# Performance work log

Measured on AMD Instinct MI355X. Metric: run time of the kernel, lower is better.

Reference implementation:

```python
import jax, jax.numpy as jnp
import numpy as np

D = 384      # d_model
NH = 8       # num_heads
HW = 96      # spatial h = w
RATIOS = (4, 8, 16)


def _p2i(x):
    # (hg wg b) c h w -> b c (hg h) (wg w), hg=wg=2, b=1
    f, c, h, w = x.shape
    return x.reshape(2, 2, c, h, w).transpose(2, 0, 3, 1, 4).reshape(1, c, 2 * h, 2 * w)


def _i2p(x):
    # b c (hg h) (wg w) -> (hg wg b) c h w, hg=wg=2, b=1
    _, c, H2, W2 = x.shape
    h, w = H2 // 2, W2 // 2
    return x.reshape(c, 2, h, 2, w).transpose(1, 3, 0, 2, 4).reshape(4, c, h, w)


def _ln(x, g, b, eps=1e-5):
    m = x.mean(-1, keepdims=True)
    v = ((x - m) ** 2).mean(-1, keepdims=True)
    return (x - m) * jax.lax.rsqrt(v + eps) * g + b


def setup_inputs() -> dict:
    key = jax.random.key(0)
    ks = jax.random.split(key, 8)
    rn = lambda k, s: jax.random.normal(k, s, dtype=jnp.float32) * 0.02
    return {
        "x": jax.random.normal(ks[0], (5, D, HW, HW), dtype=jnp.float32),
        "sal_w": rn(ks[1], (1, D)),
        "sal_b": jnp.zeros((1,), jnp.float32),
        "attn_in_w": rn(ks[2], (4, 3 * D, D)),
        "attn_in_b": jnp.zeros((4, 3 * D), jnp.float32),
        "attn_out_w": rn(ks[3], (4, D, D)),
        "attn_out_b": jnp.zeros((4, D), jnp.float32),
        "w3": rn(ks[4], (2 * D, D)),
        "b3": jnp.zeros((2 * D,), jnp.float32),
        "w4": rn(ks[5], (D, 2 * D)),
        "b4": jnp.zeros((D,), jnp.float32),
        "g1": jnp.ones((D,), jnp.float32),
        "be1": jnp.zeros((D,), jnp.float32),
        "g2": jnp.ones((D,), jnp.float32),
        "be2": jnp.zeros((D,), jnp.float32),
    }


def reference(x, sal_w, sal_b, attn_in_w, attn_in_b, attn_out_w, attn_out_b,
              w3, b3, w4, b4, g1, be1, g2, be2):
    b, c, h, w = x.shape
    loc, glb = x[:4], x[4:5]                      # (4,c,h,w), (1,c,h,w)
    pg = _i2p(glb)                                # (4,c,h/2,w/2)

    tam = jax.nn.sigmoid(jnp.einsum('oc,chw->ohw', sal_w, glb[0]) + sal_b[:, None, None])  # (1,h,w)
    tam_up = jnp.repeat(jnp.repeat(tam, 2, axis=1), 2, axis=2)[None]                        # (1,1,2h,2w)
    loc = loc * _i2p(tam_up)                      # (4,c,h,w) * (4,1,h,w)

    # multi-ratio adaptive average pooling of patched global (sizes divide exactly)
    pools = []
    for r in RATIOS:
        th, tw = round(h / r), round(w / r)
        kh, kw = (h // 2) // th, (w // 2) // tw
        p = pg.reshape(4, c, th, kh, tw, kw).mean((3, 5))
        pools.append(p.reshape(4, c, th * tw))
    kv = jnp.concatenate(pools, axis=2).transpose(0, 2, 1)   # (4,S,c)

    q = loc.reshape(4, c, h * w).transpose(0, 2, 1)          # (4,L,c)

    # 4 independent MHA blocks, vectorized over the patch dim n
    dh = c // NH
    wq, wk, wv = attn_in_w[:, :c], attn_in_w[:, c:2 * c], attn_in_w[:, 2 * c:]
    bq, bk, bv = attn_in_b[:, :c], attn_in_b[:, c:2 * c], attn_in_b[:, 2 * c:]
    heads = lambda t: t.reshape(4, -1, NH, dh).transpose(0, 2, 1, 3)
    qh = heads(jnp.einsum('nlc,ndc->nld', q, wq) + bq[:, None, :])
    kh = heads(jnp.einsum('nsc,ndc->nsd', kv, wk) + bk[:, None, :])
    vh = heads(jnp.einsum('nsc,ndc->nsd', kv, wv) + bv[:, None, :])
    scores = jnp.einsum('nhld,nhsd->nhls', qh, kh) / jnp.sqrt(jnp.float32(dh))
    attn = jax.nn.softmax(scores, axis=-1)
    ao = jnp.einsum('nhls,nhsd->nhld', attn, vh).transpose(0, 2, 1, 3).reshape(4, -1, c)
    ao = jnp.einsum('nlc,ndc->nld', ao, attn_out_w) + attn_out_b[:, None, :]  # (4,L,c)
    outputs = ao.transpose(1, 0, 2)                                           # (L,4,c)

    # residual + FFN block (dropouts are identity in eval)
    src = loc.reshape(4, c, -1).transpose(2, 0, 1) + outputs                  # (L,4,c)
    src = _ln(src, g1, be1)
    hid = jax.nn.gelu(jnp.einsum('lnc,dc->lnd', src, w3) + b3, approximate=False)
    ff = jnp.einsum('lnd,cd->lnc', hid, w4) + b4
    src = _ln(src + ff, g2, be2)
    src = src.transpose(1, 2, 0).reshape(4, c, h, w)

    # nearest-downsample (factor 2) of stitched patches, add to global
    glb = glb + _p2i(src)[:, :, ::2, ::2]
    return jnp.concatenate([src, glb], axis=0)
```

## Files before the change

### kernel.cpp

```cpp
#include <hip/hip_runtime.h>

typedef __attribute__((ext_vector_type(8))) __bf16 bf16x8;
typedef __attribute__((ext_vector_type(4))) __bf16 bf16x4;
typedef __attribute__((ext_vector_type(4))) float f32x4;

__device__ __forceinline__ bf16x8 zero8() {
  bf16x8 z;
#pragma unroll
  for (int i = 0; i < 8; ++i) z[i] = (__bf16)0.f;
  return z;
}

__device__ __forceinline__ float wave_sum(float v) {
#pragma unroll
  for (int off = 1; off < 64; off <<= 1) v += __shfl_xor(v, off);
  return v;
}

__global__ __launch_bounds__(256) void k_cvt(const float* __restrict__ in,
    __bf16* __restrict__ o, int n4) {
  const int i = blockIdx.x * 256 + threadIdx.x;
  if (i < n4) {
    const f32x4 v = ((const f32x4*)in)[i];
    bf16x4 b;
#pragma unroll
    for (int e = 0; e < 4; ++e) b[e] = (__bf16)v[e];
    ((bf16x4*)o)[i] = b;
  }
}

__global__ __launch_bounds__(256) void k_tam(const float* __restrict__ x,
    const float* __restrict__ sal_w, const float* __restrict__ sal_b,
    float* __restrict__ tam) {
  const int lane = threadIdx.x & 63, w = threadIdx.x >> 6;
  const int pix = blockIdx.x * 64 + lane;
  const float* g = x + (size_t)4 * 384 * 9216;
  float acc = 0.f;
  for (int c = w * 96; c < w * 96 + 96; ++c)
    acc += sal_w[c] * g[(size_t)c * 9216 + pix];
  __shared__ float part[4][64];
  part[w][lane] = acc;
  __syncthreads();
  if (w == 0) {
    float v = part[0][lane] + part[1][lane] + part[2][lane] + part[3][lane] + sal_b[0];
    tam[pix] = 1.f / (1.f + __expf(-v));
  }
}

__global__ __launch_bounds__(256) void k_locscale(const float* __restrict__ x,
    const float* __restrict__ tam, __bf16* __restrict__ Q) {
  const int n = blockIdx.y;
  const int l0 = blockIdx.x * 64;
  const int tid = threadIdx.x;
  __shared__ float tile[64][69];
  const size_t bx = (size_t)n * 384 * 9216;
  const int a = n >> 1, b = n & 1;
  for (int c0 = 0; c0 < 384; c0 += 64) {
    if (c0) __syncthreads();
#pragma unroll
    for (int pass = 0; pass < 4; ++pass) {
      int cc = pass * 16 + (tid >> 4);
      int ll = (tid & 15) * 4;
      f32x4 v = *(const f32x4*)&x[bx + (size_t)(c0 + cc) * 9216 + l0 + ll];
#pragma unroll
      for (int e = 0; e < 4; ++e) tile[cc][ll + e] = v[e];
    }
    __syncthreads();
    const int ll = tid >> 2, c1 = (tid & 3) * 16;
    const int l = l0 + ll, i = l / 96, j = l % 96;
    const float tv = tam[(a * 48 + (i >> 1)) * 96 + b * 48 + (j >> 1)];
    const size_t orow = ((size_t)n * 9216 + l) * 384 + c0 + c1;
#pragma unroll
    for (int cc = 0; cc < 16; ++cc)
      Q[orow + cc] = (__bf16)(tile[c1 + cc][ll] * tv);
  }
}

__global__ __launch_bounds__(64) void k_pool(const float* __restrict__ x,
    __bf16* __restrict__ KV) {
  const int c = blockIdx.x, n = blockIdx.y;
  const int a = n >> 1, b = n & 1;
  const float* g = x + (size_t)(4 * 384 + c) * 9216;
  __shared__ float quad[48][48];
  const int t = threadIdx.x;
  for (int k = t; k < 2304; k += 64) {
    int i = k / 48, j = k % 48;
    quad[i][j] = g[(a * 48 + i) * 96 + b * 48 + j];
  }
  __syncthreads();
  for (int s = t; s < 768; s += 64) {
    float val = 0.f;
    if (s < 576) {
      int ti = s / 24, tj = s % 24;
#pragma unroll
      for (int di = 0; di < 2; ++di)
#pragma unroll
        for (int dj = 0; dj < 2; ++dj) val += quad[ti * 2 + di][tj * 2 + dj];
      val *= 0.25f;
    } else if (s < 720) {
      int q = s - 576; int ti = q / 12, tj = q % 12;
      for (int di = 0; di < 4; ++di)
        for (int dj = 0; dj < 4; ++dj) val += quad[ti * 4 + di][tj * 4 + dj];
      val *= (1.f / 16.f);
    } else if (s < 756) {
      int q = s - 720; int ti = q / 6, tj = q % 6;
      for (int di = 0; di < 8; ++di)
        for (int dj = 0; dj < 8; ++dj) val += quad[ti * 8 + di][tj * 8 + dj];
      val *= (1.f / 64.f);
    }
    KV[((size_t)n * 768 + s) * 384 + c] = (__bf16)val;
  }
}

template <int GELU>
__global__ __launch_bounds__(256) void k_gemm(const __bf16* __restrict__ A,
    const __bf16* __restrict__ B, const float* __restrict__ bias,
    __bf16* __restrict__ C, int K, long sA, long sB, long sBias, long sC,
    float scale) {
  const int z = blockIdx.z;
  A += (size_t)z * sA; B += (size_t)z * sB; bias += (size_t)z * sBias; C += (size_t)z * sC;
  const int m0 = blockIdx.y * 128, n0 = blockIdx.x * 128;
  const int N = gridDim.x * 128;
  __shared__ __bf16 As[128 * 64], Bs[128 * 64];
  const int tid = threadIdx.x, lane = tid & 63, w = tid >> 6;
  const int wm = w >> 1, wn = w & 1;
  const int li = lane & 15, gq = lane >> 4;
  const int lrow = lane >> 3, lcol = (lane & 7) * 8;
  f32x4 acc[4][4] = {};
  const int nk = K >> 6;
  for (int kt = 0; kt < nk; ++kt) {
    const int k0 = kt * 64;
#pragma unroll
    for (int i = 0; i < 4; ++i) {
      const int r0 = w * 32 + i * 8;
      const __bf16* ga = A + (size_t)(m0 + r0 + lrow) * K + k0 + lcol;
      const __bf16* gb = B + (size_t)(n0 + r0 + lrow) * K + k0 + lcol;
      __builtin_amdgcn_global_load_lds(
          (const __attribute__((address_space(1))) void*)ga,
          (__attribute__((address_space(3))) void*)&As[r0 * 64], 16, 0, 0);
      __builtin_amdgcn_global_load_lds(
          (const __attribute__((address_space(1))) void*)gb,
          (__attribute__((address_space(3))) void*)&Bs[r0 * 64], 16, 0, 0);
    }
    __syncthreads();
#pragma unroll
    for (int kk = 0; kk < 2; ++kk) {
      bf16x8 af[4], bfr[4];
#pragma unroll
      for (int f = 0; f < 4; ++f) {
        af[f] = *(const bf16x8*)&As[(wm * 64 + f * 16 + li) * 64 + kk * 32 + gq * 8];
        bfr[f] = *(const bf16x8*)&Bs[(wn * 64 + f * 16 + li) * 64 + kk * 32 + gq * 8];
      }
#pragma unroll
      for (int fm = 0; fm < 4; ++fm)
#pragma unroll
        for (int fn = 0; fn < 4; ++fn)
          acc[fm][fn] = __builtin_amdgcn_mfma_f32_16x16x32_bf16(af[fm], bfr[fn], acc[fm][fn], 0, 0, 0);
    }
    __syncthreads();
  }
  float bv[4];
#pragma unroll
  for (int fn = 0; fn < 4; ++fn) bv[fn] = bias[n0 + wn * 64 + fn * 16 + li];
#pragma unroll
  for (int fm = 0; fm < 4; ++fm) {
    const int row = m0 + wm * 64 + fm * 16 + gq * 4;
#pragma unroll
    for (int fn = 0; fn < 4; ++fn) {
      const int col = n0 + wn * 64 + fn * 16 + li;
#pragma unroll
      for (int r = 0; r < 4; ++r) {
        float v = (acc[fm][fn][r] + bv[fn]) * scale;
        if (GELU) v = 0.5f * v * (1.f + erff(v * 0.70710678118654752f));
        C[(size_t)(row + r) * N + col] = (__bf16)v;
      }
    }
  }
}

__global__ __launch_bounds__(256) void k_vt(const __bf16* __restrict__ VH,
    __bf16* __restrict__ VT) {
  const int nh = blockIdx.y, n = nh >> 3, h = nh & 7;
  const int s0 = blockIdx.x * 256;
  __shared__ __bf16 tile[48][264];
  const int tid = threadIdx.x;
  const size_t bv = ((size_t)n * 768) * 384 + h * 48;
#pragma unroll
  for (int it = 0; it < 6; ++it) {
    const int task = tid + it * 256;
    const int s = task / 6, ch = task % 6;
    bf16x8 v = *(const bf16x8*)&VH[bv + (size_t)(s0 + s) * 384 + ch * 8];
#pragma unroll
    for (int e = 0; e < 8; ++e) tile[ch * 8 + e][s] = v[e];
  }
  __syncthreads();
#pragma unroll
  for (int it = 0; it < 6; ++it) {
    const int task = tid + it * 256;
    const int d = task >> 5, so = (task & 31) * 8;
    bf16x8 v2 = *(const bf16x8*)&tile[d][so];
    *(bf16x8*)&VT[((size_t)nh * 48 + d) * 768 + s0 + so] = v2;
  }
}

__global__ __launch_bounds__(256) void k_attn(const __bf16* __restrict__ QH,
    const __bf16* __restrict__ KH, const __bf16* __restrict__ VT,
    __bf16* __restrict__ AO) {
  const int nh = blockIdx.y, n = nh >> 3, h = nh & 7;
  const int l0 = blockIdx.x * 64;
  const int tid = threadIdx.x, lane = tid & 63, w = tid >> 6;
  const int gq = lane >> 4, li = lane & 15;
  const int l0w = l0 + w * 16;
  __shared__ __bf16 Ks[64 * 64];
  __shared__ __bf16 Vs[48 * 64];
  __shared__ __bf16 P[4][16 * 68];
  __bf16* Pw = &P[w][0];
  const size_t bq = ((size_t)n * 9216) * 384 + h * 48;
  const size_t bk = ((size_t)n * 768) * 384 + h * 48;
  const __bf16* vt = VT + (size_t)nh * 48 * 768;
  const int scol = 8 * ((lane & 7) ^ (lane >> 3));
  const int rsw = 8 * (li & 7);
  bf16x8 qf[2];
#pragma unroll
  for (int kk = 0; kk < 2; ++kk) {
    const int d0 = kk * 32 + gq * 8;
    qf[kk] = (d0 < 48) ? *(const bf16x8*)&QH[bq + (size_t)(l0w + li) * 384 + d0] : zero8();
  }
  float m_run = -1e30f, l_run = 0.f;
  f32x4 o[3] = {};
  for (int t = 0; t < 12; ++t) {
    const int s0 = t * 64;
    __syncthreads();
#pragma unroll
    for (int j = 0; j < 2; ++j) {
      const int rbase = w * 16 + j * 8;
      const __bf16* src = KH + bk + (size_t)(s0 + rbase + (lane >> 3)) * 384 + scol;
      __builtin_amdgcn_global_load_lds(
          (const __attribute__((address_space(1))) void*)src,
          (__attribute__((address_space(3))) void*)&Ks[rbase * 64], 16, 0, 0);
    }
    for (int j = w; j < 6; j += 4) {
      const int rbase = j * 8;
      const __bf16* src = vt + (size_t)(rbase + (lane >> 3)) * 768 + s0 + scol;
      __builtin_amdgcn_global_load_lds(
          (const __attribute__((address_space(1))) void*)src,
          (__attribute__((address_space(3))) void*)&Vs[rbase * 64], 16, 0, 0);
    }
    __syncthreads();
    f32x4 sc[4];
#pragma unroll
    for (int st = 0; st < 4; ++st) {
      f32x4 a = {};
#pragma unroll
      for (int kk = 0; kk < 2; ++kk) {
        const bf16x8 kf = *(const bf16x8*)&Ks[(st * 16 + li) * 64 + ((kk * 32 + gq * 8) ^ rsw)];
        a = __builtin_amdgcn_mfma_f32_16x16x32_bf16(kf, qf[kk], a, 0, 0, 0);
      }
      sc[st] = a;
    }
    if (t == 11) {
#pragma unroll
      for (int st = 0; st < 4; ++st)
#pragma unroll
        for (int r = 0; r < 4; ++r)
          if (st * 16 + gq * 4 + r >= 52) sc[st][r] = -1e30f;
    }
    float mloc = -1e30f;
#pragma unroll
    for (int st = 0; st < 4; ++st)
      mloc = fmaxf(mloc, fmaxf(fmaxf(sc[st][0], sc[st][1]), fmaxf(sc[st][2], sc[st][3])));
    mloc = fmaxf(mloc, __shfl_xor(mloc, 16));
    mloc = fmaxf(mloc, __shfl_xor(mloc, 32));
    const float m_new = fmaxf(m_run, mloc);
    const float alpha = __builtin_amdgcn_exp2f(m_run - m_new);
    float psum = 0.f;
#pragma unroll
    for (int st = 0; st < 4; ++st)
#pragma unroll
      for (int r = 0; r < 4; ++r) {
        const float p = __builtin_amdgcn_exp2f(sc[st][r] - m_new);
        sc[st][r] = p;
        psum += p;
      }
    psum += __shfl_xor(psum, 16);
    psum += __shfl_xor(psum, 32);
    l_run = l_run * alpha + psum;
    m_run = m_new;
    float ar[4];
#pragma unroll
    for (int r = 0; r < 4; ++r) ar[r] = __shfl(alpha, gq * 4 + r, 16);
#pragma unroll
    for (int df = 0; df < 3; ++df)
#pragma unroll
      for (int r = 0; r < 4; ++r) o[df][r] *= ar[r];
#pragma unroll
    for (int st = 0; st < 4; ++st) {
      bf16x4 pk;
#pragma unroll
      for (int r = 0; r < 4; ++r) pk[r] = (__bf16)sc[st][r];
      *(bf16x4*)&Pw[li * 68 + st * 16 + gq * 4] = pk;
    }
#pragma unroll
    for (int kk = 0; kk < 2; ++kk) {
      const bf16x4 plo = *(const bf16x4*)&Pw[li * 68 + kk * 32 + gq * 8];
      const bf16x4 phi = *(const bf16x4*)&Pw[li * 68 + kk * 32 + gq * 8 + 4];
      bf16x8 ap;
#pragma unroll
      for (int e = 0; e < 4; ++e) { ap[e] = plo[e]; ap[e + 4] = phi[e]; }
#pragma unroll
      for (int df = 0; df < 3; ++df) {
        const bf16x8 bv = *(const bf16x8*)&Vs[(df * 16 + li) * 64 + ((kk * 32 + gq * 8) ^ rsw)];
        o[df] = __builtin_amdgcn_mfma_f32_16x16x32_bf16(ap, bv, o[df], 0, 0, 0);
      }
    }
  }
  const float inv = 1.f / l_run;
  float ir[4];
#pragma unroll
  for (int r = 0; r < 4; ++r) ir[r] = __shfl(inv, gq * 4 + r, 16);
#pragma unroll
  for (int df = 0; df < 3; ++df)
#pragma unroll
    for (int r = 0; r < 4; ++r)
      AO[bq + (size_t)(l0w + gq * 4 + r) * 384 + df * 16 + li] = (__bf16)(o[df][r] * ir[r]);
}

__global__ __launch_bounds__(256) void k_ln1(const __bf16* Q,
    const __bf16* P, const float* g1, const float* b1, __bf16* S1) {
  const size_t row = (size_t)blockIdx.x * 4 + (threadIdx.x >> 6);
  const int lane = threadIdx.x & 63;
  const __bf16* q = Q + row * 384;
  const __bf16* p = P + row * 384;
  float v[6], s = 0.f;
#pragma unroll
  for (int e = 0; e < 6; ++e) {
    const int c = e * 64 + lane;
    v[e] = (float)q[c] + (float)p[c];
    s += v[e];
  }
  s = wave_sum(s);
  const float mean = s * (1.f / 384.f);
  float var = 0.f;
#pragma unroll
  for (int e = 0; e < 6; ++e) { const float d = v[e] - mean; var += d * d; }
  var = wave_sum(var) * (1.f / 384.f);
  const float rstd = rsqrtf(var + 1e-5f);
  __bf16* o = S1 + row * 384;
#pragma unroll
  for (int e = 0; e < 6; ++e) {
    const int c = e * 64 + lane;
    o[c] = (__bf16)(((v[e] - mean) * rstd) * g1[c] + b1[c]);
  }
}

__global__ __launch_bounds__(256) void k_ln2(const __bf16* __restrict__ S1,
    const __bf16* __restrict__ FF, const float* __restrict__ g2,
    const float* __restrict__ b2, float* __restrict__ out) {
  const int n = blockIdx.y, l0 = blockIdx.x * 64;
  const int tid = threadIdx.x, w = tid >> 6, lane = tid & 63;
  __shared__ __bf16 tile[64][390];
  for (int rr = 0; rr < 16; ++rr) {
    const int ll = w * 16 + rr;
    const size_t row = ((size_t)n * 9216 + l0 + ll) * 384;
    float v[6], s = 0.f;
#pragma unroll
    for (int e = 0; e < 6; ++e) {
      const int c = e * 64 + lane;
      v[e] = (float)S1[row + c] + (float)FF[row + c];
      s += v[e];
    }
    s = wave_sum(s);
    const float mean = s * (1.f / 384.f);
    float var = 0.f;
#pragma unroll
    for (int e = 0; e < 6; ++e) { const float d = v[e] - mean; var += d * d; }
    var = wave_sum(var) * (1.f / 384.f);
    const float rstd = rsqrtf(var + 1e-5f);
#pragma unroll
    for (int e = 0; e < 6; ++e) {
      const int c = e * 64 + lane;
      tile[ll][c] = (__bf16)(((v[e] - mean) * rstd) * g2[c] + b2[c]);
    }
  }
  __syncthreads();
  for (int it = 0; it < 96; ++it) {
    const int c = it * 4 + w;
    out[((size_t)n * 384 + c) * 9216 + l0 + lane] = (float)tile[lane][c];
  }
}

__global__ __launch_bounds__(256) void k_glb(const float* __restrict__ x,
    float* out) {
  const int gl = blockIdx.x * 64 + (threadIdx.x & 63);
  const int c = blockIdx.y * 4 + (threadIdx.x >> 6);
  const int y = gl / 96, xx = gl % 96;
  const int np = ((y / 48) << 1) + (xx / 48);
  const int ls = ((y % 48) * 2) * 96 + (xx % 48) * 2;
  const float v = x[(size_t)(4 * 384 + c) * 9216 + gl] +
                  out[((size_t)np * 384 + c) * 9216 + ls];
  out[(size_t)(4 * 384 + c) * 9216 + gl] = v;
}

extern "C" void kernel_launch(void* const* d_in, const int* in_sizes, int n_in,
                              void* d_out, int out_size, void* d_ws, size_t ws_size,
                              hipStream_t stream) {
  const float* x     = (const float*)d_in[0];
  const float* sal_w = (const float*)d_in[1];
  const float* sal_b = (const float*)d_in[2];
  const float* aiw   = (const float*)d_in[3];
  const float* aib   = (const float*)d_in[4];
  const float* aow   = (const float*)d_in[5];
  const float* aob   = (const float*)d_in[6];
  const float* w3    = (const float*)d_in[7];
  const float* b3    = (const float*)d_in[8];
  const float* w4    = (const float*)d_in[9];
  const float* b4    = (const float*)d_in[10];
  const float* g1    = (const float*)d_in[11];
  const float* be1   = (const float*)d_in[12];
  const float* g2    = (const float*)d_in[13];
  const float* be2   = (const float*)d_in[14];
  float* out = (float*)d_out;
  char* ws = (char*)d_ws;

  float*  tam  = (float*)(ws + 0);
  __bf16* aiwB = (__bf16*)(ws + 36864);
  __bf16* aowB = (__bf16*)(ws + 3575808);
  __bf16* w3B  = (__bf16*)(ws + 4755456);
  __bf16* w4B  = (__bf16*)(ws + 5345280);
  __bf16* KV   = (__bf16*)(ws + 5935104);
  __bf16* KHb  = (__bf16*)(ws + 8294400);
  __bf16* VHb  = (__bf16*)(ws + 10653696);
  __bf16* Q    = (__bf16*)(ws + 13012992);
  __bf16* QHb  = (__bf16*)(ws + 41324544);
  __bf16* VTg = KV;
  __bf16* AO  = (__bf16*)d_out;
  __bf16* HID = (__bf16*)d_out;
  __bf16* P   = QHb;
  __bf16* S1  = Q;
  __bf16* FF  = QHb;

  const float qscale = 0.20823509f;

  k_cvt<<<1728, 256, 0, stream>>>(aiw, aiwB, 442368);
  k_cvt<<<576, 256, 0, stream>>>(aow, aowB, 147456);
  k_cvt<<<288, 256, 0, stream>>>(w3, w3B, 73728);
  k_cvt<<<288, 256, 0, stream>>>(w4, w4B, 73728);

  k_tam<<<144, 256, 0, stream>>>(x, sal_w, sal_b, tam);
  k_locscale<<<dim3(144, 4), 256, 0, stream>>>(x, tam, Q);
  k_pool<<<dim3(384, 4), 64, 0, stream>>>(x, KV);

  k_gemm<0><<<dim3(3, 6, 4), 256, 0, stream>>>(KV, aiwB + 384 * 384, aib + 384, KHb,
      384, 768L * 384, 1152L * 384, 1152L, 768L * 384, 1.f);
  k_gemm<0><<<dim3(3, 6, 4), 256, 0, stream>>>(KV, aiwB + 768 * 384, aib + 768, VHb,
      384, 768L * 384, 1152L * 384, 1152L, 768L * 384, 1.f);
  k_gemm<0><<<dim3(3, 72, 4), 256, 0, stream>>>(Q, aiwB, aib, QHb,
      384, 9216L * 384, 1152L * 384, 1152L, 9216L * 384, qscale);

  k_vt<<<dim3(3, 32), 256, 0, stream>>>(VHb, VTg);

  k_attn<<<dim3(144, 32), 256, 0, stream>>>(QHb, KHb, VTg, AO);

  k_gemm<0><<<dim3(3, 72, 4), 256, 0, stream>>>(AO, aowB, aob, P,
      384, 9216L * 384, 384L * 384, 384L, 9216L * 384, 1.f);

  k_ln1<<<9216, 256, 0, stream>>>(Q, P, g1, be1, S1);

  k_gemm<1><<<dim3(6, 288, 1), 256, 0, stream>>>(S1, w3B, b3, HID,
      384, 0, 0, 0, 0, 1.f);
  k_gemm<0><<<dim3(3, 288, 1), 256, 0, stream>>>(HID, w4B, b4, FF,
      768, 0, 0, 0, 0, 1.f);

  k_ln2<<<dim3(144, 4), 256, 0, stream>>>(S1, FF, g2, be2, out);
  k_glb<<<dim3(144, 96), 256, 0, stream>>>(x, out);
}
```

Before: 383.6 us.

## Replace online softmax max with Cauchy-Schwarz bound; fuse K/V projection and weight casts

```diff
diff --git a/kernel.cpp b/kernel.cpp
--- a/kernel.cpp
+++ b/kernel.cpp
@@ -17,16 +17,22 @@
   return v;
 }
 
-__global__ __launch_bounds__(256) void k_cvt(const float* __restrict__ in,
-    __bf16* __restrict__ o, int n4) {
+__global__ __launch_bounds__(256) void k_cvt4(const float* __restrict__ a,
+    const float* __restrict__ b, const float* __restrict__ c, const float* __restrict__ d,
+    __bf16* __restrict__ oa, __bf16* __restrict__ ob, __bf16* __restrict__ oc,
+    __bf16* __restrict__ od) {
   const int i = blockIdx.x * 256 + threadIdx.x;
-  if (i < n4) {
-    const f32x4 v = ((const f32x4*)in)[i];
-    bf16x4 b;
-#pragma unroll
-    for (int e = 0; e < 4; ++e) b[e] = (__bf16)v[e];
-    ((bf16x4*)o)[i] = b;
-  }
+  const float* src; __bf16* dst; int off;
+  if (i < 442368)      { src = a; dst = oa; off = i; }
+  else if (i < 589824) { src = b; dst = ob; off = i - 442368; }
+  else if (i < 663552) { src = c; dst = oc; off = i - 589824; }
+  else if (i < 737280) { src = d; dst = od; off = i - 663552; }
+  else return;
+  const f32x4 v = ((const f32x4*)src)[off];
+  bf16x4 o;
+#pragma unroll
+  for (int e = 0; e < 4; ++e) o[e] = (__bf16)v[e];
+  ((bf16x4*)dst)[off] = o;
 }
 
 __global__ __launch_bounds__(256) void k_tam(const float* __restrict__ x,
@@ -178,18 +184,42 @@
   }
 }
 
-__global__ __launch_bounds__(256) void k_vt(const __bf16* __restrict__ VH,
+__global__ __launch_bounds__(256) void k_kmax(const __bf16* __restrict__ KVH,
+    float* __restrict__ kmax) {
+  const int nh = blockIdx.x, n = nh >> 3, h = nh & 7;
+  const size_t bk = (size_t)n * 768 * 768 + h * 48;
+  const int tid = threadIdx.x;
+  float m = 0.f;
+  for (int s = tid; s < 756; s += 256) {
+    float a2 = 0.f;
+#pragma unroll
+    for (int ch = 0; ch < 6; ++ch) {
+      bf16x8 kv = *(const bf16x8*)&KVH[bk + (size_t)s * 768 + ch * 8];
+#pragma unroll
+      for (int e = 0; e < 8; ++e) { const float f = (float)kv[e]; a2 += f * f; }
+    }
+    m = fmaxf(m, a2);
+  }
+#pragma unroll
+  for (int off = 1; off < 64; off <<= 1) m = fmaxf(m, __shfl_xor(m, off));
+  __shared__ float red[4];
+  if ((tid & 63) == 0) red[tid >> 6] = m;
+  __syncthreads();
+  if (tid == 0) kmax[nh] = fmaxf(fmaxf(red[0], red[1]), fmaxf(red[2], red[3]));
+}
+
+__global__ __launch_bounds__(256) void k_vt(const __bf16* __restrict__ KVH,
     __bf16* __restrict__ VT) {
   const int nh = blockIdx.y, n = nh >> 3, h = nh & 7;
   const int s0 = blockIdx.x * 256;
   __shared__ __bf16 tile[48][264];
   const int tid = threadIdx.x;
-  const size_t bv = ((size_t)n * 768) * 384 + h * 48;
+  const size_t bv = (size_t)n * 768 * 768 + 384 + h * 48;
 #pragma unroll
   for (int it = 0; it < 6; ++it) {
     const int task = tid + it * 256;
     const int s = task / 6, ch = task % 6;
-    bf16x8 v = *(const bf16x8*)&VH[bv + (size_t)(s0 + s) * 384 + ch * 8];
+    bf16x8 v = *(const bf16x8*)&KVH[bv + (size_t)(s0 + s) * 768 + ch * 8];
 #pragma unroll
     for (int e = 0; e < 8; ++e) tile[ch * 8 + e][s] = v[e];
   }
@@ -204,8 +234,8 @@
 }
 
 __global__ __launch_bounds__(256) void k_attn(const __bf16* __restrict__ QH,
-    const __bf16* __restrict__ KH, const __bf16* __restrict__ VT,
-    __bf16* __restrict__ AO) {
+    const __bf16* __restrict__ KVH, const __bf16* __restrict__ VT,
+    const float* __restrict__ kmax, __bf16* __restrict__ AO) {
   const int nh = blockIdx.y, n = nh >> 3, h = nh & 7;
   const int l0 = blockIdx.x * 64;
   const int tid = threadIdx.x, lane = tid & 63, w = tid >> 6;
@@ -216,7 +246,7 @@
   __shared__ __bf16 P[4][16 * 68];
   __bf16* Pw = &P[w][0];
   const size_t bq = ((size_t)n * 9216) * 384 + h * 48;
-  const size_t bk = ((size_t)n * 768) * 384 + h * 48;
+  const size_t bk = (size_t)n * 768 * 768 + h * 48;
   const __bf16* vt = VT + (size_t)nh * 48 * 768;
   const int scol = 8 * ((lane & 7) ^ (lane >> 3));
   const int rsw = 8 * (li & 7);
@@ -226,7 +256,15 @@
     const int d0 = kk * 32 + gq * 8;
     qf[kk] = (d0 < 48) ? *(const bf16x8*)&QH[bq + (size_t)(l0w + li) * 384 + d0] : zero8();
   }
-  float m_run = -1e30f, l_run = 0.f;
+  float q2 = 0.f;
+#pragma unroll
+  for (int kk = 0; kk < 2; ++kk)
+#pragma unroll
+    for (int e = 0; e < 8; ++e) { const float f = (float)qf[kk][e]; q2 += f * f; }
+  q2 += __shfl_xor(q2, 16);
+  q2 += __shfl_xor(q2, 32);
+  const float m_fix = sqrtf(q2 * kmax[nh]);
+  float l_run = 0.f;
   f32x4 o[3] = {};
   for (int t = 0; t < 12; ++t) {
     const int s0 = t * 64;
@@ -234,7 +272,7 @@
 #pragma unroll
     for (int j = 0; j < 2; ++j) {
       const int rbase = w * 16 + j * 8;
-      const __bf16* src = KH + bk + (size_t)(s0 + rbase + (lane >> 3)) * 384 + scol;
+      const __bf16* src = KVH + bk + (size_t)(s0 + rbase + (lane >> 3)) * 768 + scol;
       __builtin_amdgcn_global_load_lds(
           (const __attribute__((address_space(1))) void*)src,
           (__attribute__((address_space(3))) void*)&Ks[rbase * 64], 16, 0, 0);
@@ -265,34 +303,14 @@
         for (int r = 0; r < 4; ++r)
           if (st * 16 + gq * 4 + r >= 52) sc[st][r] = -1e30f;
     }
-    float mloc = -1e30f;
 #pragma unroll
     for (int st = 0; st < 4; ++st)
-      mloc = fmaxf(mloc, fmaxf(fmaxf(sc[st][0], sc[st][1]), fmaxf(sc[st][2], sc[st][3])));
-    mloc = fmaxf(mloc, __shfl_xor(mloc, 16));
-    mloc = fmaxf(mloc, __shfl_xor(mloc, 32));
-    const float m_new = fmaxf(m_run, mloc);
-    const float alpha = __builtin_amdgcn_exp2f(m_run - m_new);
-    float psum = 0.f;
-#pragma unroll
-    for (int st = 0; st < 4; ++st)
 #pragma unroll
       for (int r = 0; r < 4; ++r) {
-        const float p = __builtin_amdgcn_exp2f(sc[st][r] - m_new);
+        const float p = __builtin_amdgcn_exp2f(sc[st][r] - m_fix);
         sc[st][r] = p;
-        psum += p;
+        l_run += p;
       }
-    psum += __shfl_xor(psum, 16);
-    psum += __shfl_xor(psum, 32);
-    l_run = l_run * alpha + psum;
-    m_run = m_new;
-    float ar[4];
-#pragma unroll
-    for (int r = 0; r < 4; ++r) ar[r] = __shfl(alpha, gq * 4 + r, 16);
-#pragma unroll
-    for (int df = 0; df < 3; ++df)
-#pragma unroll
-      for (int r = 0; r < 4; ++r) o[df][r] *= ar[r];
 #pragma unroll
     for (int st = 0; st < 4; ++st) {
       bf16x4 pk;
@@ -314,6 +332,8 @@
       }
     }
   }
+  l_run += __shfl_xor(l_run, 16);
+  l_run += __shfl_xor(l_run, 32);
   const float inv = 1.f / l_run;
   float ir[4];
 #pragma unroll
@@ -428,38 +448,34 @@
   __bf16* w3B  = (__bf16*)(ws + 4755456);
   __bf16* w4B  = (__bf16*)(ws + 5345280);
   __bf16* KV   = (__bf16*)(ws + 5935104);
-  __bf16* KHb  = (__bf16*)(ws + 8294400);
-  __bf16* VHb  = (__bf16*)(ws + 10653696);
+  __bf16* KVH  = (__bf16*)(ws + 8294400);
   __bf16* Q    = (__bf16*)(ws + 13012992);
   __bf16* QHb  = (__bf16*)(ws + 41324544);
   __bf16* VTg = KV;
   __bf16* AO  = (__bf16*)d_out;
   __bf16* HID = (__bf16*)d_out;
+  float* kmax = (float*)((char*)d_out + 70778368);
   __bf16* P   = QHb;
   __bf16* S1  = Q;
   __bf16* FF  = QHb;
 
   const float qscale = 0.20823509f;
 
-  k_cvt<<<1728, 256, 0, stream>>>(aiw, aiwB, 442368);
-  k_cvt<<<576, 256, 0, stream>>>(aow, aowB, 147456);
-  k_cvt<<<288, 256, 0, stream>>>(w3, w3B, 73728);
-  k_cvt<<<288, 256, 0, stream>>>(w4, w4B, 73728);
+  k_cvt4<<<2880, 256, 0, stream>>>(aiw, aow, w3, w4, aiwB, aowB, w3B, w4B);
 
   k_tam<<<144, 256, 0, stream>>>(x, sal_w, sal_b, tam);
   k_locscale<<<dim3(144, 4), 256, 0, stream>>>(x, tam, Q);
   k_pool<<<dim3(384, 4), 64, 0, stream>>>(x, KV);
 
-  k_gemm<0><<<dim3(3, 6, 4), 256, 0, stream>>>(KV, aiwB + 384 * 384, aib + 384, KHb,
-      384, 768L * 384, 1152L * 384, 1152L, 768L * 384, 1.f);
-  k_gemm<0><<<dim3(3, 6, 4), 256, 0, stream>>>(KV, aiwB + 768 * 384, aib + 768, VHb,
-      384, 768L * 384, 1152L * 384, 1152L, 768L * 384, 1.f);
+  k_gemm<0><<<dim3(6, 6, 4), 256, 0, stream>>>(KV, aiwB + 384 * 384, aib + 384, KVH,
+      384, 768L * 384, 1152L * 384, 1152L, 768L * 768, 1.f);
   k_gemm<0><<<dim3(3, 72, 4), 256, 0, stream>>>(Q, aiwB, aib, QHb,
       384, 9216L * 384, 1152L * 384, 1152L, 9216L * 384, qscale);
 
-  k_vt<<<dim3(3, 32), 256, 0, stream>>>(VHb, VTg);
-
-  k_attn<<<dim3(144, 32), 256, 0, stream>>>(QHb, KHb, VTg, AO);
+  k_kmax<<<32, 256, 0, stream>>>(KVH, kmax);
+  k_vt<<<dim3(3, 32), 256, 0, stream>>>(KVH, VTg);
+
+  k_attn<<<dim3(144, 32), 256, 0, stream>>>(QHb, KVH, VTg, kmax, AO);
 
   k_gemm<0><<<dim3(3, 72, 4), 256, 0, stream>>>(AO, aowB, aob, P,
       384, 9216L * 384, 384L * 384, 384L, 9216L * 384, 1.f);
```

New measurement: 360.5 us. -6.0%, faster.
